# Optimization experiments

Measured on AMD Instinct MI355X. Metric: run time of the kernel, lower is better.

The kernel has to match this reference:

```python
import jax, jax.numpy as jnp
import numpy as np

B, S, D_IN, D_OUT, H = 2, 2048, 1024, 1024, 16
HD = D_OUT // H  # head dim = 64


def setup_inputs() -> dict:
    key = jax.random.key(0)
    ks = jax.random.split(key, 9)
    s_in = 1.0 / np.sqrt(D_IN)
    s_out = 1.0 / np.sqrt(D_OUT)
    return {
        "X": jax.random.normal(ks[0], (B, S, D_IN), dtype=jnp.float32),
        "Wq": jax.random.uniform(ks[1], (D_OUT, D_IN), jnp.float32, -s_in, s_in),
        "bq": jax.random.uniform(ks[2], (D_OUT,), jnp.float32, -s_in, s_in),
        "Wk": jax.random.uniform(ks[3], (D_OUT, D_IN), jnp.float32, -s_in, s_in),
        "bk": jax.random.uniform(ks[4], (D_OUT,), jnp.float32, -s_in, s_in),
        "Wv": jax.random.uniform(ks[5], (D_OUT, D_IN), jnp.float32, -s_in, s_in),
        "bv": jax.random.uniform(ks[6], (D_OUT,), jnp.float32, -s_in, s_in),
        "Wo": jax.random.uniform(ks[7], (D_OUT, D_OUT), jnp.float32, -s_out, s_out),
        "bo": jax.random.uniform(ks[8], (D_OUT,), jnp.float32, -s_out, s_out),
    }


def reference(X, Wq, bq, Wk, bk, Wv, bv, Wo, bo):
    scale = jnp.asarray(HD ** 0.5, X.dtype)  # self.dim = sqrt(head_dim)
    q = X @ Wq.T + bq  # [B,S,D_OUT]
    k = X @ Wk.T + bk
    v = X @ Wv.T + bv
    # split heads: b s (h d) -> b h s d
    q = q.reshape(B, S, H, HD).transpose(0, 2, 1, 3)
    k = k.reshape(B, S, H, HD).transpose(0, 2, 1, 3)
    v = v.reshape(B, S, H, HD).transpose(0, 2, 1, 3)
    scores = jnp.einsum('bhsd,bhtd->bhst', q, k) / scale  # [B,H,S,S]
    causal = jnp.triu(jnp.ones((S, S), dtype=bool), k=1)
    scores = jnp.where(causal, -jnp.inf, scores)
    weights = jax.nn.softmax(scores, axis=-1)
    out = jnp.einsum('bhst,bhtd->bhsd', weights, v)  # [B,H,S,HD]
    out = out.transpose(0, 2, 1, 3).reshape(B, S, D_OUT)  # b h s d -> b s (h d)
    return out @ Wo.T + bo
```

## Files before the change

### kernel.cpp

```cpp
#include <hip/hip_runtime.h>
#include <hip/hip_bf16.h>

typedef __bf16 bf16_t;
typedef __bf16 bf16x8 __attribute__((ext_vector_type(8)));
typedef float  f32x4  __attribute__((ext_vector_type(4)));
typedef unsigned short ushort_t;

#define MFMA16(a, b, c) __builtin_amdgcn_mfma_f32_16x16x32_bf16((a), (b), (c), 0, 0, 0)
#define GLDS16(g, l) __builtin_amdgcn_global_load_lds( \
    (const __attribute__((address_space(1))) unsigned int*)(g), \
    (__attribute__((address_space(3))) unsigned int*)(l), 16, 0, 0)

#define WAITCNT_VM(n)  (0x0F70 | (n))
#define WAITCNT_LGKM0  0xC07F

#define MEMFENCE asm volatile("" ::: "memory")

#define SWZ(r) ((((r) >> 1) ^ ((r) >> 3)) & 3)

#define QSCALE 0.18033688f

__global__ __launch_bounds__(256) void cvt_all(
    const void* __restrict__ X,  const void* __restrict__ W0, const void* __restrict__ W1,
    const void* __restrict__ W2, const void* __restrict__ W3,
    const void* __restrict__ c0, const void* __restrict__ c1,
    const void* __restrict__ c2, const void* __restrict__ c3,
    bf16_t* __restrict__ Xb, bf16_t* __restrict__ Wb, float* __restrict__ biasF,
    int* __restrict__ flag)
{
    const int tid  = threadIdx.x;
    const int lane = tid & 63;
    const ushort_t u = ((const ushort_t*)X)[2 * lane];
    const int e = (u >> 7) & 0xFF;
    const int f = (__ballot(e >= 0xA0) != 0ull) ? 1 : 0;

    const int bid = blockIdx.x;
    if (bid >= 4096) {
        if (bid == 4096 && tid == 0) *flag = f;
        const int idx = ((bid - 4096) * 256 + tid) * 8;
        const int w = idx >> 10, off = idx & 1023;
        const void* src = (w == 0) ? c0 : (w == 1) ? c1 : (w == 2) ? c2 : c3;
        #pragma unroll
        for (int r = 0; r < 8; ++r)
            biasF[idx + r] = f ? ((const float*)src)[off + r]
                               : (float)((const bf16_t*)src)[off + r];
        return;
    }

    const long long i = (long long)bid * 2048 + tid * 8;
    const void* src;
    bf16_t* dst;
    long long off;
    if (i < 4194304) { src = X; dst = Xb; off = i; }
    else {
        const int w = (int)((i - 4194304) >> 20);
        off = (i - 4194304) & 1048575;
        src = (w == 0) ? W0 : (w == 1) ? W1 : (w == 2) ? W2 : W3;
        dst = Wb + (size_t)w * 1048576;
    }
    if (f) {
        const float* s = (const float*)src + off;
        const float4 a = *(const float4*)(s);
        const float4 b = *(const float4*)(s + 4);
        bf16x8 o;
        o[0] = (bf16_t)a.x; o[1] = (bf16_t)a.y; o[2] = (bf16_t)a.z; o[3] = (bf16_t)a.w;
        o[4] = (bf16_t)b.x; o[5] = (bf16_t)b.y; o[6] = (bf16_t)b.z; o[7] = (bf16_t)b.w;
        *(bf16x8*)(dst + off) = o;
    } else {
        *(bf16x8*)(dst + off) = *(const bf16x8*)((const bf16_t*)src + off);
    }
}

__global__ __launch_bounds__(512, 2) void gemm_qkv(
    const bf16_t* __restrict__ A,
    const bf16_t* __restrict__ Wst,
    const float* __restrict__ biasAll,
    bf16_t* __restrict__ C, bf16_t* __restrict__ Vt)
{
    __shared__ bf16_t Ash[4][256 * 32];
    __shared__ bf16_t Bsh[4][192 * 32];

    const int tid  = threadIdx.x;
    const int wid  = tid >> 6;
    const int lane = tid & 63;
    const int g    = lane >> 4;
    const int c    = lane & 15;

    const int m0 = blockIdx.x * 256;
    const int n0 = blockIdx.y * 192;

    const int srow = lane >> 2;
    const int sblk = (lane & 3) ^ ((lane >> 3) & 3);
    const bf16_t* Ag  = A   + (size_t)(m0 + wid * 32 + srow) * 1024 + sblk * 8;
    const bf16_t* Wg0 = Wst + (size_t)(n0 + wid * 16 + srow) * 1024 + sblk * 8;
    const bf16_t* Wg1 = Wst + (size_t)(n0 + 128 + wid * 16 + srow) * 1024 + sblk * 8;

    const int waveM = (wid >> 2) * 128;
    const int waveN = (wid & 3) * 48;
    const int fblk  = (g ^ ((c >> 1) & 3)) * 8;

    f32x4 acc[8][3] = {};

    auto stage = [&](int H) {
        const int buf = H & 3;
        GLDS16(Ag + H * 32,                      &Ash[buf][(wid * 32) * 32]);
        GLDS16(Ag + (size_t)16 * 1024 + H * 32,  &Ash[buf][(wid * 32 + 16) * 32]);
        GLDS16(Wg0 + H * 32,                     &Bsh[buf][(wid * 16) * 32]);
        if (wid < 4)
            GLDS16(Wg1 + H * 32,                 &Bsh[buf][(128 + wid * 16) * 32]);
    };

    stage(0); stage(1); stage(2);
    if (wid < 4) __builtin_amdgcn_s_waitcnt(WAITCNT_VM(8));
    else         __builtin_amdgcn_s_waitcnt(WAITCNT_VM(6));
    __builtin_amdgcn_s_barrier();
    MEMFENCE;

    #pragma unroll 4
    for (int H = 0; H < 32; ++H) {
        const int buf = H & 3;
        const bf16_t* As = Ash[buf];
        const bf16_t* Bs = Bsh[buf];

        bf16x8 bfr[3], af[8];
        #pragma unroll
        for (int j = 0; j < 3; ++j)
            bfr[j] = *(const bf16x8*)(&Bs[(waveN + j * 16 + c) * 32 + fblk]);
        #pragma unroll
        for (int i = 0; i < 8; ++i)
            af[i] = *(const bf16x8*)(&As[(waveM + i * 16 + c) * 32 + fblk]);

        if (H < 29) stage(H + 3);

        __builtin_amdgcn_s_setprio(1);
        #pragma unroll
        for (int i = 0; i < 8; ++i)
            #pragma unroll
            for (int j = 0; j < 3; ++j)
                acc[i][j] = MFMA16(af[i], bfr[j], acc[i][j]);
        __builtin_amdgcn_s_setprio(0);

        MEMFENCE;
        __builtin_amdgcn_s_waitcnt(WAITCNT_LGKM0);
        if (H < 29) {
            if (wid < 4) __builtin_amdgcn_s_waitcnt(WAITCNT_VM(8));
            else         __builtin_amdgcn_s_waitcnt(WAITCNT_VM(6));
        } else if (H == 29) {
            if (wid < 4) __builtin_amdgcn_s_waitcnt(WAITCNT_VM(4));
            else         __builtin_amdgcn_s_waitcnt(WAITCNT_VM(3));
        } else if (H == 30) {
            __builtin_amdgcn_s_waitcnt(WAITCNT_VM(0));
        }
        __builtin_amdgcn_s_barrier();
        MEMFENCE;
    }

    #pragma unroll
    for (int j = 0; j < 3; ++j) {
        const int cg0 = n0 + waveN + j * 16;
        const int col = cg0 + c;
        const float bv = biasAll[col];
        if (cg0 >= 2048) {
            const int hcol = col - 2048;
            const int h = hcol >> 6, d = hcol & 63;
            #pragma unroll
            for (int i = 0; i < 8; ++i) {
                const int row = m0 + waveM + i * 16 + g * 4;
                const int bb = row >> 11, s = row & 2047;
                bf16_t pk[4];
                #pragma unroll
                for (int r = 0; r < 4; ++r) pk[r] = (bf16_t)(acc[i][j][r] + bv);
                *(uint2*)(&Vt[(((size_t)bb * 16 + h) * 64 + d) * 2048 + s]) = *(uint2*)pk;
            }
        } else {
            const float os = (cg0 < 1024) ? QSCALE : 1.0f;
            #pragma unroll
            for (int i = 0; i < 8; ++i) {
                const int row = m0 + waveM + i * 16 + g * 4;
                #pragma unroll
                for (int r = 0; r < 4; ++r)
                    C[(size_t)(row + r) * 3072 + col] = (bf16_t)((acc[i][j][r] + bv) * os);
            }
        }
    }
}

__global__ __launch_bounds__(512, 1) void gemm_op(
    const bf16_t* __restrict__ A,
    const bf16_t* __restrict__ W,
    const float* __restrict__ bs,
    void* __restrict__ C,
    const int* __restrict__ flag)
{
    __shared__ bf16_t As[3][2][128 * 32];
    __shared__ bf16_t Bs[3][2][128 * 32];

    const int f32out = *flag;

    const int tid  = threadIdx.x;
    const int wid  = tid >> 6;
    const int lane = tid & 63;
    const int g    = lane >> 4;
    const int c    = lane & 15;

    const int m0 = blockIdx.x * 128;
    const int n0 = blockIdx.y * 128;

    const int srow = lane >> 2;
    const int sblk = (lane & 3) ^ ((lane >> 3) & 3);
    const bf16_t* Ag = A + (size_t)(m0 + wid * 16 + srow) * 1024 + sblk * 8;
    const bf16_t* Wg = W + (size_t)(n0 + wid * 16 + srow) * 1024 + sblk * 8;

    const int waveM = (wid >> 2) * 64;
    const int waveN = (wid & 3) * 32;
    const int fblk  = (g ^ ((c >> 1) & 3)) * 8;

    f32x4 acc[4][2] = {};

    auto stage = [&](int t) {
        const int buf = t % 3;
        const size_t k0 = (size_t)t * 64;
        GLDS16(Ag + k0,      &As[buf][0][(wid * 16) * 32]);
        GLDS16(Ag + k0 + 32, &As[buf][1][(wid * 16) * 32]);
        GLDS16(Wg + k0,      &Bs[buf][0][(wid * 16) * 32]);
        GLDS16(Wg + k0 + 32, &Bs[buf][1][(wid * 16) * 32]);
    };

    stage(0); stage(1);
    __builtin_amdgcn_s_waitcnt(WAITCNT_VM(4));
    __builtin_amdgcn_s_barrier();
    MEMFENCE;

    #pragma unroll 3
    for (int s = 0; s < 16; ++s) {
        const int buf = s % 3;

        if (s < 14) stage(s + 2);

        __builtin_amdgcn_s_setprio(1);
        #pragma unroll
        for (int kh = 0; kh < 2; ++kh) {
            bf16x8 af[4], bfr[2];
            #pragma unroll
            for (int i = 0; i < 4; ++i)
                af[i] = *(const bf16x8*)(&As[buf][kh][(waveM + i * 16 + c) * 32 + fblk]);
            #pragma unroll
            for (int j = 0; j < 2; ++j)
                bfr[j] = *(const bf16x8*)(&Bs[buf][kh][(waveN + j * 16 + c) * 32 + fblk]);
            #pragma unroll
            for (int i = 0; i < 4; ++i)
                #pragma unroll
                for (int j = 0; j < 2; ++j)
                    acc[i][j] = MFMA16(af[i], bfr[j], acc[i][j]);
        }
        __builtin_amdgcn_s_setprio(0);

        MEMFENCE;
        __builtin_amdgcn_s_waitcnt(WAITCNT_LGKM0);
        if (s < 14)       __builtin_amdgcn_s_waitcnt(WAITCNT_VM(4));
        else if (s == 14) __builtin_amdgcn_s_waitcnt(WAITCNT_VM(0));
        __builtin_amdgcn_s_barrier();
        MEMFENCE;
    }

    #pragma unroll
    for (int j = 0; j < 2; ++j) {
        const int col = n0 + waveN + j * 16 + c;
        const float bv = bs[col];
        #pragma unroll
        for (int i = 0; i < 4; ++i) {
            const int row = m0 + waveM + i * 16 + g * 4;
            #pragma unroll
            for (int r = 0; r < 4; ++r) {
                const float val = acc[i][j][r] + bv;
                const size_t idx = (size_t)(row + r) * 1024 + col;
                if (f32out) ((float*)C)[idx] = val;
                else        ((bf16_t*)C)[idx] = (bf16_t)val;
            }
        }
    }
}

__global__ __launch_bounds__(256, 4) void attn_kernel(
    const bf16_t* __restrict__ QKV, const bf16_t* __restrict__ Vt,
    bf16_t* __restrict__ O)
{
    __shared__ bf16_t Ksh[2][64][32];
    __shared__ bf16_t Vsh[2][64][32];
    __shared__ bf16_t Psh[4][16][72];

    const int tid  = threadIdx.x;
    const int wid  = tid >> 6;
    const int lane = tid & 63;
    const int g    = lane >> 4;
    const int c    = lane & 15;

    const int bh = blockIdx.y;
    const int b  = bh >> 4, h = bh & 15;
    const int qt = (bh < 16) ? blockIdx.x : (31 - blockIdx.x);
    const int q0 = qt * 64;
    const int nt = qt + 1;

    bf16x8 aq[2];
    {
        const bf16_t* qp = QKV + (size_t)(b * 2048 + q0 + wid * 16 + c) * 3072 + h * 64;
        aq[0] = *(const bf16x8*)(qp + g * 8);
        aq[1] = *(const bf16x8*)(qp + 32 + g * 8);
    }

    float li = 0.0f;
    f32x4 o2[4] = {};

    const int sr = tid >> 2;
    const int j4 = tid & 3;
    const bf16_t* Kg = QKV + (size_t)(b * 2048 + sr) * 3072 + 1024 + h * 64 + j4 * 8;
    const bf16_t* Vg = Vt + ((size_t)bh * 64 + sr) * 2048 + j4 * 8;

    const int sp = (j4 ^ SWZ(sr)) * 8;
    bf16_t* kd0 = &Ksh[0][sr][sp];
    bf16_t* kd1 = &Ksh[1][sr][sp];
    bf16_t* vd0 = &Vsh[0][sr][sp];
    bf16_t* vd1 = &Vsh[1][sr][sp];

    uint4 kr0 = *(const uint4*)(Kg);
    uint4 kr1 = *(const uint4*)(Kg + 32);
    uint4 vr0 = *(const uint4*)(Vg);
    uint4 vr1 = *(const uint4*)(Vg + 32);

    const int qg = q0 + wid * 16 + c;

    for (int jt = 0; jt < nt; ++jt) {
        *(uint4*)kd0 = kr0;
        *(uint4*)kd1 = kr1;
        *(uint4*)vd0 = vr0;
        *(uint4*)vd1 = vr1;
        __syncthreads();

        if (jt + 1 < nt) {
            const size_t ko = (size_t)(jt + 1) * 64 * 3072;
            kr0 = *(const uint4*)(Kg + ko);
            kr1 = *(const uint4*)(Kg + ko + 32);
            vr0 = *(const uint4*)(Vg + (jt + 1) * 64);
            vr1 = *(const uint4*)(Vg + (jt + 1) * 64 + 32);
        }

        f32x4 s[4] = {};
        __builtin_amdgcn_s_setprio(1);
        #pragma unroll
        for (int n = 0; n < 4; ++n)
            #pragma unroll
            for (int kb = 0; kb < 2; ++kb) {
                const int row = n * 16 + c;
                const bf16x8 kf = *(const bf16x8*)(&Ksh[kb][row][(g ^ SWZ(row)) * 8]);
                s[n] = MFMA16(kf, aq[kb], s[n]);
            }
        __builtin_amdgcn_s_setprio(0);

        if (jt == nt - 1) {
            const int j0 = jt * 64;
            #pragma unroll
            for (int n = 0; n < 4; ++n)
                #pragma unroll
                for (int r = 0; r < 4; ++r)
                    if (j0 + n * 16 + g * 4 + r > qg) s[n][r] = -1e30f;
        }

        #pragma unroll
        for (int n = 0; n < 4; ++n) {
            const float p0 = __builtin_amdgcn_exp2f(s[n][0]);
            const float p1 = __builtin_amdgcn_exp2f(s[n][1]);
            const float p2 = __builtin_amdgcn_exp2f(s[n][2]);
            const float p3 = __builtin_amdgcn_exp2f(s[n][3]);
            li += (p0 + p1) + (p2 + p3);
            union { bf16_t h[4]; uint2 u; } pk;
            pk.h[0] = (bf16_t)p0; pk.h[1] = (bf16_t)p1;
            pk.h[2] = (bf16_t)p2; pk.h[3] = (bf16_t)p3;
            const int pw = ((n ^ (c >> 2)) << 2) + (g ^ (c & 3));
            *(uint2*)(&Psh[wid][c][pw * 4]) = pk.u;
        }
        __builtin_amdgcn_wave_barrier();

        bf16x8 pb[2];
        #pragma unroll
        for (int kb = 0; kb < 2; ++kb) {
            const int n0  = 2 * kb + (g >> 1);
            const int gs  = (g & 1) * 2;
            const int base = ((n0 ^ (c >> 2)) << 2);
            const uint2 w0 = *(const uint2*)(&Psh[wid][c][(base + (gs ^ (c & 3))) * 4]);
            const uint2 w1 = *(const uint2*)(&Psh[wid][c][(base + ((gs + 1) ^ (c & 3))) * 4]);
            union { uint4 u; bf16x8 v; } cvt;
            cvt.u.x = w0.x; cvt.u.y = w0.y; cvt.u.z = w1.x; cvt.u.w = w1.y;
            pb[kb] = cvt.v;
        }

        __builtin_amdgcn_s_setprio(1);
        #pragma unroll
        for (int kb = 0; kb < 2; ++kb)
            #pragma unroll
            for (int dt = 0; dt < 4; ++dt) {
                const int row = dt * 16 + c;
                const bf16x8 vf = *(const bf16x8*)(&Vsh[kb][row][(g ^ SWZ(row)) * 8]);
                o2[dt] = MFMA16(vf, pb[kb], o2[dt]);
            }
        __builtin_amdgcn_s_setprio(0);
        __syncthreads();
    }

    li += __shfl_xor(li, 16, 64);
    li += __shfl_xor(li, 32, 64);
    const float inv = 1.0f / li;

    const size_t orow = (size_t)(b * 2048 + q0 + wid * 16 + c);
    #pragma unroll
    for (int dt = 0; dt < 4; ++dt) {
        union { bf16_t h[4]; uint2 u; } pk;
        #pragma unroll
        for (int r = 0; r < 4; ++r) pk.h[r] = (bf16_t)(o2[dt][r] * inv);
        *(uint2*)(&O[orow * 1024 + h * 64 + dt * 16 + g * 4]) = pk.u;
    }
}

extern "C" void kernel_launch(void* const* d_in, const int* in_sizes, int n_in,
                              void* d_out, int out_size, void* d_ws, size_t ws_size,
                              hipStream_t stream)
{
    const void* X  = d_in[0];
    const void* Wq = d_in[1];  const void* bq = d_in[2];
    const void* Wk = d_in[3];  const void* bk = d_in[4];
    const void* Wv = d_in[5];  const void* bv = d_in[6];
    const void* Wo = d_in[7];  const void* bo = d_in[8];

    int*    flag  = (int*)d_ws;
    float*  biasF = (float*)((char*)d_ws + 16);
    bf16_t* Xb    = (bf16_t*)((char*)d_ws + 16 + 16384);
    bf16_t* Wb    = Xb  + (size_t)4096 * 1024;
    bf16_t* QKV   = Wb  + (size_t)4 * 1024 * 1024;
    bf16_t* Vt    = QKV + (size_t)4096 * 3072;
    bf16_t* Ao    = Vt  + (size_t)4096 * 1024;

    const size_t MW = (size_t)1024 * 1024;

    cvt_all<<<4098, 256, 0, stream>>>(X, Wq, Wk, Wv, Wo, bq, bk, bv, bo,
                                      Xb, Wb, biasF, flag);

    gemm_qkv<<<dim3(16, 16), 512, 0, stream>>>(Xb, Wb, biasF, QKV, Vt);
    attn_kernel<<<dim3(32, 32), 256, 0, stream>>>(QKV, Vt, Ao);
    gemm_op<<<dim3(32, 8), 512, 0, stream>>>(
        Ao, Wb + 3 * MW, biasF + 3072, d_out, flag);
}
```

Before: 186.7 us.

## Double-buffer K/V tiles in LDS and pass P via lane shuffles

The attention loop now keeps two LDS buffers for K and V. The next tile is written into the alternate buffer after the PV MFMAs, which removes one of the two __syncthreads per iteration. The probability matrix P is no longer staged through a per-wave LDS scratch area; it is rearranged into the MFMA B-operand layout with __shfl cross-lane permutes instead. This trades LDS round-trips and a barrier for extra ds_bpermute shuffles and select instructions, and doubles the K/V LDS footprint, which could affect occupancy.

```diff
diff --git a/kernel.cpp b/kernel.cpp
--- a/kernel.cpp
+++ b/kernel.cpp
@@ -5,6 +5,7 @@
 typedef __bf16 bf16x8 __attribute__((ext_vector_type(8)));
 typedef float  f32x4  __attribute__((ext_vector_type(4)));
 typedef unsigned short ushort_t;
+typedef unsigned int uint_t;
 
 #define MFMA16(a, b, c) __builtin_amdgcn_mfma_f32_16x16x32_bf16((a), (b), (c), 0, 0, 0)
 #define GLDS16(g, l) __builtin_amdgcn_global_load_lds( \
@@ -285,9 +286,8 @@
     const bf16_t* __restrict__ QKV, const bf16_t* __restrict__ Vt,
     bf16_t* __restrict__ O)
 {
-    __shared__ bf16_t Ksh[2][64][32];
-    __shared__ bf16_t Vsh[2][64][32];
-    __shared__ bf16_t Psh[4][16][72];
+    __shared__ bf16_t Ksh[2][2][64][32];
+    __shared__ bf16_t Vsh[2][2][64][32];
 
     const int tid  = threadIdx.x;
     const int wid  = tid >> 6;
@@ -317,24 +317,22 @@
     const bf16_t* Vg = Vt + ((size_t)bh * 64 + sr) * 2048 + j4 * 8;
 
     const int sp = (j4 ^ SWZ(sr)) * 8;
-    bf16_t* kd0 = &Ksh[0][sr][sp];
-    bf16_t* kd1 = &Ksh[1][sr][sp];
-    bf16_t* vd0 = &Vsh[0][sr][sp];
-    bf16_t* vd1 = &Vsh[1][sr][sp];
 
     uint4 kr0 = *(const uint4*)(Kg);
     uint4 kr1 = *(const uint4*)(Kg + 32);
     uint4 vr0 = *(const uint4*)(Vg);
     uint4 vr1 = *(const uint4*)(Vg + 32);
 
+    *(uint4*)(&Ksh[0][0][sr][sp]) = kr0;
+    *(uint4*)(&Ksh[0][1][sr][sp]) = kr1;
+    *(uint4*)(&Vsh[0][0][sr][sp]) = vr0;
+    *(uint4*)(&Vsh[0][1][sr][sp]) = vr1;
+    __syncthreads();
+
     const int qg = q0 + wid * 16 + c;
 
     for (int jt = 0; jt < nt; ++jt) {
-        *(uint4*)kd0 = kr0;
-        *(uint4*)kd1 = kr1;
-        *(uint4*)vd0 = vr0;
-        *(uint4*)vd1 = vr1;
-        __syncthreads();
+        const int cur = jt & 1;
 
         if (jt + 1 < nt) {
             const size_t ko = (size_t)(jt + 1) * 64 * 3072;
@@ -351,7 +349,7 @@
             #pragma unroll
             for (int kb = 0; kb < 2; ++kb) {
                 const int row = n * 16 + c;
-                const bf16x8 kf = *(const bf16x8*)(&Ksh[kb][row][(g ^ SWZ(row)) * 8]);
+                const bf16x8 kf = *(const bf16x8*)(&Ksh[cur][kb][row][(g ^ SWZ(row)) * 8]);
                 s[n] = MFMA16(kf, aq[kb], s[n]);
             }
         __builtin_amdgcn_s_setprio(0);
@@ -365,6 +363,7 @@
                     if (j0 + n * 16 + g * 4 + r > qg) s[n][r] = -1e30f;
         }
 
+        uint_t pk[4][2];
         #pragma unroll
         for (int n = 0; n < 4; ++n) {
             const float p0 = __builtin_amdgcn_exp2f(s[n][0]);
@@ -372,25 +371,31 @@
             const float p2 = __builtin_amdgcn_exp2f(s[n][2]);
             const float p3 = __builtin_amdgcn_exp2f(s[n][3]);
             li += (p0 + p1) + (p2 + p3);
-            union { bf16_t h[4]; uint2 u; } pk;
-            pk.h[0] = (bf16_t)p0; pk.h[1] = (bf16_t)p1;
-            pk.h[2] = (bf16_t)p2; pk.h[3] = (bf16_t)p3;
-            const int pw = ((n ^ (c >> 2)) << 2) + (g ^ (c & 3));
-            *(uint2*)(&Psh[wid][c][pw * 4]) = pk.u;
-        }
-        __builtin_amdgcn_wave_barrier();
+            union { bf16_t h[2]; uint_t u; } t0, t1;
+            t0.h[0] = (bf16_t)p0; t0.h[1] = (bf16_t)p1;
+            t1.h[0] = (bf16_t)p2; t1.h[1] = (bf16_t)p3;
+            pk[n][0] = t0.u; pk[n][1] = t1.u;
+        }
 
         bf16x8 pb[2];
+        const int src0 = c + ((lane & 16) << 1);
+        const bool hi_g = (lane & 32) != 0;
         #pragma unroll
         for (int kb = 0; kb < 2; ++kb) {
-            const int n0  = 2 * kb + (g >> 1);
-            const int gs  = (g & 1) * 2;
-            const int base = ((n0 ^ (c >> 2)) << 2);
-            const uint2 w0 = *(const uint2*)(&Psh[wid][c][(base + (gs ^ (c & 3))) * 4]);
-            const uint2 w1 = *(const uint2*)(&Psh[wid][c][(base + ((gs + 1) ^ (c & 3))) * 4]);
-            union { uint4 u; bf16x8 v; } cvt;
-            cvt.u.x = w0.x; cvt.u.y = w0.y; cvt.u.z = w1.x; cvt.u.w = w1.y;
-            pb[kb] = cvt.v;
+            uint_t w[4];
+            #pragma unroll
+            for (int bsel = 0; bsel < 2; ++bsel) {
+                const int src = src0 + bsel * 16;
+                const uint_t lo0 = __shfl((int)pk[2 * kb][0], src, 64);
+                const uint_t hi0 = __shfl((int)pk[2 * kb][1], src, 64);
+                const uint_t lo1 = __shfl((int)pk[2 * kb + 1][0], src, 64);
+                const uint_t hi1 = __shfl((int)pk[2 * kb + 1][1], src, 64);
+                w[2 * bsel]     = hi_g ? lo1 : lo0;
+                w[2 * bsel + 1] = hi_g ? hi1 : hi0;
+            }
+            union { uint_t u[4]; bf16x8 v; } cvt_;
+            cvt_.u[0] = w[0]; cvt_.u[1] = w[1]; cvt_.u[2] = w[2]; cvt_.u[3] = w[3];
+            pb[kb] = cvt_.v;
         }
 
         __builtin_amdgcn_s_setprio(1);
@@ -399,10 +404,17 @@
             #pragma unroll
             for (int dt = 0; dt < 4; ++dt) {
                 const int row = dt * 16 + c;
-                const bf16x8 vf = *(const bf16x8*)(&Vsh[kb][row][(g ^ SWZ(row)) * 8]);
+                const bf16x8 vf = *(const bf16x8*)(&Vsh[cur][kb][row][(g ^ SWZ(row)) * 8]);
                 o2[dt] = MFMA16(vf, pb[kb], o2[dt]);
             }
         __builtin_amdgcn_s_setprio(0);
+
+        if (jt + 1 < nt) {
+            *(uint4*)(&Ksh[cur ^ 1][0][sr][sp]) = kr0;
+            *(uint4*)(&Ksh[cur ^ 1][1][sr][sp]) = kr1;
+            *(uint4*)(&Vsh[cur ^ 1][0][sr][sp]) = vr0;
+            *(uint4*)(&Vsh[cur ^ 1][1][sr][sp]) = vr1;
+        }
         __syncthreads();
     }
 
@@ -413,10 +425,10 @@
     const size_t orow = (size_t)(b * 2048 + q0 + wid * 16 + c);
     #pragma unroll
     for (int dt = 0; dt < 4; ++dt) {
-        union { bf16_t h[4]; uint2 u; } pk;
-        #pragma unroll
-        for (int r = 0; r < 4; ++r) pk.h[r] = (bf16_t)(o2[dt][r] * inv);
-        *(uint2*)(&O[orow * 1024 + h * 64 + dt * 16 + g * 4]) = pk.u;
+        union { bf16_t h[4]; uint2 u; } pkk;
+        #pragma unroll
+        for (int r = 0; r < 4; ++r) pkk.h[r] = (bf16_t)(o2[dt][r] * inv);
+        *(uint2*)(&O[orow * 1024 + h * 64 + dt * 16 + g * 4]) = pkk.u;
     }
 }
 
```

Result: slower. 199.1 us (+6.7%).
